# Kernel tuning notes

Measured on AMD Instinct MI355X. Metric: run time of the kernel, lower is better.

Reference implementation:

```python
import jax, jax.numpy as jnp
import numpy as np

EPS = 1e-6
TEMPERATURE = 0.1
NEG_INF = -1.0e9

B, S, H = 8, 1024, 1024
M = 16384  # memory_size


def setup_inputs() -> dict:
    key = jax.random.key(0)
    ks = jax.random.split(key, 10)
    sc = 1.0 / np.sqrt(H)
    return {
        "hidden_states": jax.random.normal(ks[0], (B, S, H), jnp.float32),
        "Wk": jax.random.normal(ks[1], (H, H), jnp.float32) * sc,
        "bk": jax.random.normal(ks[2], (H,), jnp.float32) * 0.01,
        "Wv": jax.random.normal(ks[3], (H, H), jnp.float32) * sc,
        "bv": jax.random.normal(ks[4], (H,), jnp.float32) * 0.01,
        "Wo": jax.random.normal(ks[5], (H, H), jnp.float32) * sc,
        "bo": jax.random.normal(ks[6], (H,), jnp.float32) * 0.01,
        "memory_keys": jax.random.normal(ks[7], (M, H), jnp.float32),
        "memory_values": jax.random.normal(ks[8], (M, H), jnp.float32),
        "memory_usage": jax.random.randint(ks[9], (M,), 0, 3, jnp.int32),
    }


def _normalize(x):
    # matches torch: x * rsqrt(sum(x^2) + 1e-6)
    return x * jax.lax.rsqrt(jnp.sum(jnp.square(x), axis=-1, keepdims=True) + EPS)


def reference(hidden_states, Wk, bk, Wv, bv, Wo, bo,
              memory_keys, memory_values, memory_usage):
    # key projection + L2-ish normalization of queries
    q = hidden_states @ Wk.T + bk              # [B,S,H]
    qn = _normalize(q)
    mkn = _normalize(memory_keys)              # [M,H]
    # cosine-similarity attention over memory slots
    scores = jnp.einsum('bsh,mh->bsm', qn, mkn) / TEMPERATURE  # [B,S,M]
    mask = (memory_usage > 0).astype(scores.dtype)             # [M]
    scores = scores * mask + NEG_INF * (1.0 - mask)
    w = jax.nn.softmax(scores, axis=-1)                        # [B,S,M]
    retrieved = jnp.einsum('bsm,mh->bsh', w, memory_values)    # [B,S,H]
    return retrieved @ Wo.T + bo
```

## Files before the change

kernel.cpp:

```cpp
#include <hip/hip_runtime.h>
#include <hip/hip_bf16.h>
#include <stdint.h>
#include <stddef.h>

typedef __bf16 bf16_t;
typedef __attribute__((ext_vector_type(8))) __bf16 bf16x8;
typedef __attribute__((ext_vector_type(4))) __bf16 bf16x4;
typedef __attribute__((ext_vector_type(4))) float f32x4;

#define HDIM 1024
#define MSLOTS 16384
#define NROWS 8192

__device__ __forceinline__ void load16_lds(const void* g, void* l) {
  __builtin_amdgcn_global_load_lds((const __attribute__((address_space(1))) void*)g,
                                   (__attribute__((address_space(3))) void*)l, 16, 0, 0);
}

__global__ void init_compact(int* __restrict__ cmask) {
  int i = blockIdx.x * blockDim.x + threadIdx.x;
  if (i < MSLOTS) cmask[i] = 0;
}

__global__ void compact_scan(const int* __restrict__ usage, int* __restrict__ posmap,
                             int* __restrict__ cmask, int* __restrict__ smalls) {
  __shared__ int wtot[16], wbase[16];
  const int t = threadIdx.x;
  const int lane = t & 63, wid = t >> 6;
  const int base = t * 16;
  unsigned mask = 0;
  int c = 0;
  #pragma unroll
  for (int i = 0; i < 16; ++i) {
    if (usage[base + i] > 0) { mask |= (1u << i); ++c; }
  }
  int inc = c;
  #pragma unroll
  for (int d = 1; d < 64; d <<= 1) {
    int n = __shfl_up(inc, d);
    if (lane >= d) inc += n;
  }
  if (lane == 63) wtot[wid] = inc;
  __syncthreads();
  if (t == 0) {
    int acc = 0;
    #pragma unroll
    for (int w = 0; w < 16; ++w) { wbase[w] = acc; acc += wtot[w]; }
    smalls[0] = acc;
    smalls[1] = ((acc + 511) >> 9) << 9;
  }
  __syncthreads();
  int pos = wbase[wid] + inc - c;
  #pragma unroll
  for (int i = 0; i < 16; ++i) {
    if ((mask >> i) & 1u) {
      posmap[pos] = base + i;
      cmask[pos] = 1;
      ++pos;
    }
  }
}

__global__ void cvt_f32_bf16(const float* __restrict__ X, bf16_t* __restrict__ Y, int n8) {
  int i = blockIdx.x * blockDim.x + threadIdx.x;
  if (i >= n8) return;
  float4 a = ((const float4*)X)[2 * i];
  float4 b = ((const float4*)X)[2 * i + 1];
  bf16x8 o;
  o[0] = (bf16_t)a.x; o[1] = (bf16_t)a.y; o[2] = (bf16_t)a.z; o[3] = (bf16_t)a.w;
  o[4] = (bf16_t)b.x; o[5] = (bf16_t)b.y; o[6] = (bf16_t)b.z; o[7] = (bf16_t)b.w;
  ((bf16x8*)Y)[i] = o;
}

__global__ void normalize_rows(const float* __restrict__ X, bf16_t* __restrict__ Y) {
  __shared__ float part[4];
  const int t = threadIdx.x;
  const size_t row = blockIdx.x;
  float4 v = ((const float4*)(X + row * 1024))[t];
  float s = v.x * v.x + v.y * v.y + v.z * v.z + v.w * v.w;
  #pragma unroll
  for (int m = 32; m >= 1; m >>= 1) s += __shfl_xor(s, m);
  if ((t & 63) == 0) part[t >> 6] = s;
  __syncthreads();
  float tot = part[0] + part[1] + part[2] + part[3];
  float r = rsqrtf(tot + 1e-6f);
  bf16x4 o;
  o[0] = (bf16_t)(v.x * r); o[1] = (bf16_t)(v.y * r);
  o[2] = (bf16_t)(v.z * r); o[3] = (bf16_t)(v.w * r);
  *(bf16x4*)&Y[row * 1024 + t * 4] = o;
}

__global__ void normalize_gather(const float* __restrict__ mk, const int* __restrict__ posmap,
                                 const int* __restrict__ smalls, bf16_t* __restrict__ cmkn) {
  __shared__ float part[4];
  const int p = blockIdx.x;
  const int cnt = smalls[0], mpad = smalls[1];
  if (p >= mpad) return;
  const int t = threadIdx.x;
  if (p >= cnt) {
    bf16x4 z;
    z[0] = z[1] = z[2] = z[3] = (bf16_t)0.f;
    *(bf16x4*)&cmkn[(size_t)p * 1024 + t * 4] = z;
    return;
  }
  const int slot = posmap[p];
  float4 v = ((const float4*)(mk + (size_t)slot * 1024))[t];
  float s = v.x * v.x + v.y * v.y + v.z * v.z + v.w * v.w;
  #pragma unroll
  for (int m = 32; m >= 1; m >>= 1) s += __shfl_xor(s, m);
  if ((t & 63) == 0) part[t >> 6] = s;
  __syncthreads();
  float tot = part[0] + part[1] + part[2] + part[3];
  float r = rsqrtf(tot + 1e-6f);
  bf16x4 o;
  o[0] = (bf16_t)(v.x * r); o[1] = (bf16_t)(v.y * r);
  o[2] = (bf16_t)(v.z * r); o[3] = (bf16_t)(v.w * r);
  *(bf16x4*)&cmkn[(size_t)p * 1024 + t * 4] = o;
}

__global__ void transpose_gather(const float* __restrict__ mv, const int* __restrict__ posmap,
                                 const int* __restrict__ smalls, bf16_t* __restrict__ cVt) {
  __shared__ float tile[32][33];
  const int cnt = smalls[0], mpad = smalls[1];
  const int p0 = blockIdx.y * 32;
  if (p0 >= mpad) return;
  const int tx = threadIdx.x & 31, ty = threadIdx.x >> 5;
  const int h0 = blockIdx.x * 32;
  #pragma unroll
  for (int j = 0; j < 32; j += 8) {
    const int pos = p0 + ty + j;
    float val = 0.f;
    if (pos < cnt) val = mv[(size_t)posmap[pos] * 1024 + h0 + tx];
    tile[ty + j][tx] = val;
  }
  __syncthreads();
  #pragma unroll
  for (int j = 0; j < 32; j += 8)
    cVt[(size_t)(h0 + ty + j) * MSLOTS + p0 + tx] = (bf16_t)tile[tx][ty + j];
}

__global__ void zero_f32(float* __restrict__ p, int n4) {
  int i = blockIdx.x * blockDim.x + threadIdx.x;
  if (i < n4) ((float4*)p)[i] = (float4){0.f, 0.f, 0.f, 0.f};
}

__global__ void scale_cvt(const float* __restrict__ retrf, const float* __restrict__ den,
                          bf16_t* __restrict__ out, int n4) {
  int i = blockIdx.x * blockDim.x + threadIdx.x;
  if (i >= n4) return;
  float4 s = ((const float4*)retrf)[i];
  const int row = (i * 4) >> 10;
  const float r = 1.0f / den[row];
  bf16x4 o;
  o[0] = (bf16_t)(s.x * r); o[1] = (bf16_t)(s.y * r);
  o[2] = (bf16_t)(s.z * r); o[3] = (bf16_t)(s.w * r);
  ((bf16x4*)out)[i] = o;
}

__global__ void reduce_scale(const float* __restrict__ part, size_t partStride, int ks,
                             const float* __restrict__ den, bf16_t* __restrict__ out, int n4) {
  int i = blockIdx.x * blockDim.x + threadIdx.x;
  if (i >= n4) return;
  float4 s = ((const float4*)part)[i];
  for (int k = 1; k < ks; ++k) {
    float4 t = ((const float4*)(part + (size_t)k * partStride))[i];
    s.x += t.x; s.y += t.y; s.z += t.z; s.w += t.w;
  }
  const int row = (i * 4) >> 10;
  const float r = 1.0f / den[row];
  bf16x4 o;
  o[0] = (bf16_t)(s.x * r); o[1] = (bf16_t)(s.y * r);
  o[2] = (bf16_t)(s.z * r); o[3] = (bf16_t)(s.w * r);
  ((bf16x4*)out)[i] = o;
}

template <int EPI>
__global__ __launch_bounds__(512, 2)
void gemm256(const bf16_t* __restrict__ A, const bf16_t* __restrict__ Bt,
             int ldk, int kLenIn, int ldc,
             const float* __restrict__ bias,
             const int* __restrict__ cmask,
             float* __restrict__ den,
             float* __restrict__ outf, bf16_t* __restrict__ outb,
             const int* __restrict__ smalls, int ks, size_t partStride) {
  __shared__ bf16_t lA[4][256 * 32];
  __shared__ bf16_t lB[4][256 * 32];
  const int tid = threadIdx.x;
  const int lane = tid & 63;
  const int wave = tid >> 6;
  const int wr = wave >> 2;
  const int wc = wave & 3;
  const int lr = lane & 15;
  const int lq = lane >> 4;

  int bx = blockIdx.x, by = blockIdx.y, bz = blockIdx.z;
  {
    const unsigned nx = gridDim.x, ny = gridDim.y;
    if ((ny & 7u) == 0u) {
      unsigned lin = blockIdx.x + nx * (blockIdx.y + ny * blockIdx.z);
      unsigned ylow = lin & 7u;
      lin >>= 3;
      const unsigned nyh = ny >> 3;
      unsigned yhigh = lin % nyh;
      lin /= nyh;
      bx = lin % nx;
      bz = lin / nx;
      by = ylow + 8u * yhigh;
    }
  }

  int kLen = kLenIn;
  int kstart = 0;
  if (EPI == 1) {
    if (bx * 256 >= smalls[1]) return;
  }
  if (EPI == 3 || EPI == 4) {
    kLen = smalls[1] / ks;
    kstart = bz * kLen;
  }
  const int nt = kLen >> 5;

  const int srow = tid >> 2;
  const int scol = (tid & 3) * 8;
  const bf16_t* pA0 = A + (size_t)(by * 256 + srow) * ldk + kstart + scol;
  const bf16_t* pA1 = pA0 + (size_t)128 * ldk;
  const bf16_t* pB0 = Bt + (size_t)(bx * 256 + srow) * ldk + kstart + scol;
  const bf16_t* pB1 = pB0 + (size_t)128 * ldk;

  f32x4 acc[8][4];
  #pragma unroll
  for (int m = 0; m < 8; ++m)
    #pragma unroll
    for (int n = 0; n < 4; ++n) acc[m][n] = (f32x4){0.f, 0.f, 0.f, 0.f};

#define STAGE(tt)                                              \
  do {                                                         \
    const int _b = (tt) & 3;                                   \
    const size_t _ko = (size_t)(tt) * 32;                      \
    load16_lds(pA0 + _ko, &lA[_b][tid * 8]);                   \
    load16_lds(pA1 + _ko, &lA[_b][4096 + tid * 8]);            \
    load16_lds(pB0 + _ko, &lB[_b][tid * 8]);                   \
    load16_lds(pB1 + _ko, &lB[_b][4096 + tid * 8]);            \
  } while (0)

  if (nt > 0) STAGE(0);
  if (nt > 1) STAGE(1);
  if (nt > 2) STAGE(2);

  for (int t = 0; t < nt; ++t) {
    if (t + 3 < nt) STAGE(t + 3);
    const int rem = nt - 1 - t;
    if (rem >= 3)      asm volatile("s_waitcnt vmcnt(12)" ::: "memory");
    else if (rem == 2) asm volatile("s_waitcnt vmcnt(8)" ::: "memory");
    else if (rem == 1) asm volatile("s_waitcnt vmcnt(4)" ::: "memory");
    else               asm volatile("s_waitcnt vmcnt(0)" ::: "memory");
    __builtin_amdgcn_s_barrier();
    __builtin_amdgcn_sched_barrier(0);
    const int b = t & 3;
    const bf16_t* bAp = &lA[b][0];
    const bf16_t* bBp = &lB[b][0];
    bf16x8 bfr[4];
    #pragma unroll
    for (int n = 0; n < 4; ++n)
      bfr[n] = *(const bf16x8*)&bBp[(wc * 64 + n * 16 + lr) * 32 + lq * 8];
    __builtin_amdgcn_s_setprio(1);
    #pragma unroll
    for (int m = 0; m < 8; ++m) {
      bf16x8 af = *(const bf16x8*)&bAp[(wr * 128 + m * 16 + lr) * 32 + lq * 8];
      #pragma unroll
      for (int n = 0; n < 4; ++n)
        acc[m][n] = __builtin_amdgcn_mfma_f32_16x16x32_bf16(af, bfr[n], acc[m][n], 0, 0, 0);
    }
    __builtin_amdgcn_s_setprio(0);
    __builtin_amdgcn_sched_barrier(0);
    __builtin_amdgcn_s_barrier();
    __builtin_amdgcn_sched_barrier(0);
  }
#undef STAGE

  const int colBase = bx * 256 + wc * 64 + lr;
  const int rowBase = by * 256 + wr * 128 + lq * 4;

  if (EPI == 1) {
    bool ok[4];
    #pragma unroll
    for (int n = 0; n < 4; ++n) ok[n] = cmask[colBase + n * 16] > 0;
    #pragma unroll
    for (int m = 0; m < 8; ++m) {
      #pragma unroll
      for (int r = 0; r < 4; ++r) {
        const int row = rowBase + m * 16 + r;
        float s = 0.f;
        #pragma unroll
        for (int n = 0; n < 4; ++n) {
          float e = ok[n] ? exp2f(acc[m][n][r] * 14.426950408889634f) : 0.f;
          s += e;
          outb[(size_t)row * ldc + colBase + n * 16] = (bf16_t)e;
        }
        s += __shfl_xor(s, 1);
        s += __shfl_xor(s, 2);
        s += __shfl_xor(s, 4);
        s += __shfl_xor(s, 8);
        if (lr == 0) atomicAdd(&den[row], s);
      }
    }
  }
  if (EPI == 3 || EPI == 4) {
    if (EPI == 4) outf += (size_t)bz * partStride;
    #pragma unroll
    for (int m = 0; m < 8; ++m)
      #pragma unroll
      for (int n = 0; n < 4; ++n)
        #pragma unroll
        for (int r = 0; r < 4; ++r) {
          const size_t idx = (size_t)(rowBase + m * 16 + r) * ldc + colBase + n * 16;
          if (EPI == 3) atomicAdd(&outf[idx], acc[m][n][r]);
          else outf[idx] = acc[m][n][r];
        }
  }
}

template <int EPI>
__global__ void gemm_bt(const bf16_t* __restrict__ A, const bf16_t* __restrict__ Bt,
                        int ldk, int kLenIn, int ldc,
                        const float* __restrict__ bias,
                        const int* __restrict__ cmask,
                        float* __restrict__ den,
                        float* __restrict__ outf, bf16_t* __restrict__ outb,
                        const int* __restrict__ smalls, int ks, size_t partStride) {
  __shared__ bf16_t lA[128 * 32];
  __shared__ bf16_t lB[128 * 32];
  const int t = threadIdx.x;
  const int lane = t & 63;
  const int wave = t >> 6;
  const int wm = (wave >> 1) << 6;
  const int wn = (wave & 1) << 6;
  const int lr = lane & 15;
  const int lq = lane >> 4;

  int bx = blockIdx.x, by = blockIdx.y, bz = blockIdx.z;
  {
    const unsigned nx = gridDim.x, ny = gridDim.y;
    if ((ny & 7u) == 0u) {
      unsigned lin = blockIdx.x + nx * (blockIdx.y + ny * blockIdx.z);
      unsigned ylow = lin & 7u;
      lin >>= 3;
      const unsigned nyh = ny >> 3;
      unsigned yhigh = lin % nyh;
      lin /= nyh;
      bx = lin % nx;
      bz = lin / nx;
      by = ylow + 8u * yhigh;
    }
  }

  int kLen = kLenIn;
  int kstart = 0;

  const int r0 = t >> 2;
  const int c0 = (t & 3) * 8;
  const bf16_t* pA0 = A + (size_t)(by * 128 + r0) * ldk + kstart + c0;
  const bf16_t* pA1 = pA0 + (size_t)64 * ldk;
  const bf16_t* pB0 = Bt + (size_t)(bx * 128 + r0) * ldk + kstart + c0;
  const bf16_t* pB1 = pB0 + (size_t)64 * ldk;

  f32x4 acc[4][4];
  #pragma unroll
  for (int i = 0; i < 4; ++i)
    #pragma unroll
    for (int j = 0; j < 4; ++j) acc[i][j] = (f32x4){0.f, 0.f, 0.f, 0.f};

  for (int k0 = 0; k0 < kLen; k0 += 32) {
    __syncthreads();
    load16_lds(pA0, &lA[t * 8]);
    load16_lds(pA1, &lA[2048 + t * 8]);
    load16_lds(pB0, &lB[t * 8]);
    load16_lds(pB1, &lB[2048 + t * 8]);
    pA0 += 32; pA1 += 32; pB0 += 32; pB1 += 32;
    __syncthreads();
    bf16x8 af[4], bfr[4];
    #pragma unroll
    for (int i = 0; i < 4; ++i)
      af[i] = *(const bf16x8*)&lA[(wm + i * 16 + lr) * 32 + lq * 8];
    #pragma unroll
    for (int j = 0; j < 4; ++j)
      bfr[j] = *(const bf16x8*)&lB[(wn + j * 16 + lr) * 32 + lq * 8];
    #pragma unroll
    for (int i = 0; i < 4; ++i)
      #pragma unroll
      for (int j = 0; j < 4; ++j)
        acc[i][j] = __builtin_amdgcn_mfma_f32_16x16x32_bf16(af[i], bfr[j], acc[i][j], 0, 0, 0);
  }

  const int colBase = bx * 128 + wn + lr;
  const int rowBase = by * 128 + wm + lq * 4;

  #pragma unroll
  for (int j = 0; j < 4; ++j) {
    const int col = colBase + j * 16;
    float bval = 0.f;
    if (EPI == 0) bval = bias[col];
    #pragma unroll
    for (int i = 0; i < 4; ++i) {
      const int row = rowBase + i * 16;
      #pragma unroll
      for (int r = 0; r < 4; ++r) {
        const size_t idx = (size_t)(row + r) * ldc + col;
        float v = acc[i][j][r];
        if (EPI == 0) outf[idx] = v + bval;
      }
    }
  }
}

extern "C" void kernel_launch(void* const* d_in, const int* in_sizes, int n_in,
                              void* d_out, int out_size, void* d_ws, size_t ws_size,
                              hipStream_t stream) {
  const float* hs = (const float*)d_in[0];
  const float* Wk = (const float*)d_in[1];
  const float* bk = (const float*)d_in[2];
  const float* Wo = (const float*)d_in[5];
  const float* bo = (const float*)d_in[6];
  const float* mk = (const float*)d_in[7];
  const float* mv = (const float*)d_in[8];
  const int* usage = (const int*)d_in[9];
  float* out = (float*)d_out;

  char* ws = (char*)d_ws;
  size_t off = 0;
  auto alloc = [&](size_t b) -> void* {
    void* p = ws + off;
    off += (b + 255) & ~(size_t)255;
    return p;
  };
  bf16_t* cmkn = (bf16_t*)alloc((size_t)MSLOTS * HDIM * 2);
  bf16_t* cVt = (bf16_t*)alloc((size_t)HDIM * MSLOTS * 2);
  bf16_t* qnb = (bf16_t*)alloc((size_t)NROWS * HDIM * 2);
  bf16_t* retrb = (bf16_t*)alloc((size_t)NROWS * HDIM * 2);
  bf16_t* Wob = (bf16_t*)alloc((size_t)HDIM * HDIM * 2);
  float* den = (float*)alloc((size_t)NROWS * 4);
  int* posmap = (int*)alloc((size_t)MSLOTS * 4);
  int* cmask = (int*)alloc((size_t)MSLOTS * 4);
  int* smalls = (int*)alloc(256 * 4);
  const size_t fixed = off;

  int chunk = 256, ksplit = 4, partialMode = 0;
  {
    const int cc[8] = {4096, 4096, 2048, 2048, 1024, 1024, 512, 256};
    const int kk[8] = {4, 4, 8, 8, 8, 8, 16, 4};
    const int pp[8] = {1, 0, 1, 0, 1, 0, 0, 0};
    for (int ci = 0; ci < 8; ++ci) {
      size_t outBytes = pp[ci] ? (size_t)cc[ci] * HDIM * 4 * kk[ci] : (size_t)cc[ci] * HDIM * 4;
      size_t region = (size_t)cc[ci] * MSLOTS * 2 + outBytes;
      size_t phaseA = (size_t)NROWS * HDIM * 2 + (size_t)HDIM * HDIM * 2 +
                      (size_t)NROWS * HDIM * 4 + 1024;
      if (region < phaseA) region = phaseA;
      if (fixed + region <= ws_size) {
        chunk = cc[ci]; ksplit = kk[ci]; partialMode = pp[ci];
        break;
      }
    }
  }
  bf16_t* hsb = (bf16_t*)(ws + fixed);
  bf16_t* Wkb = (bf16_t*)(ws + fixed + (size_t)NROWS * HDIM * 2);
  float* qf = (float*)(ws + fixed + (size_t)NROWS * HDIM * 2 + (size_t)HDIM * HDIM * 2);
  bf16_t* P = (bf16_t*)(ws + fixed);
  float* retrf = (float*)(ws + fixed + (size_t)chunk * MSLOTS * 2);
  const size_t partStride = (size_t)chunk * HDIM;

  init_compact<<<MSLOTS / 256, 256, 0, stream>>>(cmask);
  compact_scan<<<1, 1024, 0, stream>>>(usage, posmap, cmask, smalls);
  cvt_f32_bf16<<<(NROWS * HDIM / 8 + 255) / 256, 256, 0, stream>>>(hs, hsb, NROWS * HDIM / 8);
  cvt_f32_bf16<<<(HDIM * HDIM / 8 + 255) / 256, 256, 0, stream>>>(Wk, Wkb, HDIM * HDIM / 8);
  cvt_f32_bf16<<<(HDIM * HDIM / 8 + 255) / 256, 256, 0, stream>>>(Wo, Wob, HDIM * HDIM / 8);
  normalize_gather<<<MSLOTS, 256, 0, stream>>>(mk, posmap, smalls, cmkn);
  transpose_gather<<<dim3(HDIM / 32, MSLOTS / 32), 256, 0, stream>>>(mv, posmap, smalls, cVt);

  gemm_bt<0><<<dim3(HDIM / 128, NROWS / 128), 256, 0, stream>>>(
      hsb, Wkb, HDIM, HDIM, HDIM, bk, nullptr, nullptr, qf, nullptr, smalls, 1, 0);
  normalize_rows<<<NROWS, 256, 0, stream>>>(qf, qnb);

  for (int c = 0; c < NROWS; c += chunk) {
    zero_f32<<<(chunk / 4 + 255) / 256, 256, 0, stream>>>(den, chunk / 4);
    gemm256<1><<<dim3(MSLOTS / 256, chunk / 256), 512, 0, stream>>>(
        qnb + (size_t)c * HDIM, cmkn, HDIM, HDIM, MSLOTS, nullptr, cmask, den, nullptr, P,
        smalls, 1, 0);
    if (partialMode) {
      gemm256<4><<<dim3(HDIM / 256, chunk / 256, ksplit), 512, 0, stream>>>(
          P, cVt, MSLOTS, 0, HDIM, nullptr, nullptr, nullptr, retrf, nullptr, smalls, ksplit,
          partStride);
      reduce_scale<<<(chunk * HDIM / 4 + 255) / 256, 256, 0, stream>>>(
          retrf, partStride, ksplit, den, retrb + (size_t)c * HDIM, chunk * HDIM / 4);
    } else {
      zero_f32<<<(chunk * HDIM / 4 + 255) / 256, 256, 0, stream>>>(retrf, chunk * HDIM / 4);
      gemm256<3><<<dim3(HDIM / 256, chunk / 256, ksplit), 512, 0, stream>>>(
          P, cVt, MSLOTS, 0, HDIM, nullptr, nullptr, nullptr, retrf, nullptr, smalls, ksplit,
          0);
      scale_cvt<<<(chunk * HDIM / 4 + 255) / 256, 256, 0, stream>>>(
          retrf, den, retrb + (size_t)c * HDIM, chunk * HDIM / 4);
    }
  }

  gemm_bt<0><<<dim3(HDIM / 128, NROWS / 128), 256, 0, stream>>>(
      retrb, Wob, HDIM, HDIM, HDIM, bo, nullptr, nullptr, out, nullptr, smalls, 1, 0);
}
```

Measured before the change: 918.7 us.

## Restructure gemm256 main loop to K=64 double-buffered LDS with XOR swizzle

Rewrites the 256x256 MFMA GEMM main loop. The old version used a 4-deep ring of K=32 slices; the new one uses two K=64 buffers, splits each iteration into four quarter-phases, and issues the next tile's loads between compute steps. It also XOR-swizzles the LDS layout to cut bank conflicts on the ds_read path, and lowers the k-split for chunk 512. The aim is fewer barriers per FLOP and fewer LDS conflicts, at the cost of more barriers per iteration and added dependence on the K length being a multiple of 64. gemm_bt is also cleaned up by dropping its template and unused parameters.

```diff
diff --git a/kernel.cpp b/kernel.cpp
--- a/kernel.cpp
+++ b/kernel.cpp
@@ -174,17 +174,59 @@
   ((bf16x4*)out)[i] = o;
 }
 
+#define SB __builtin_amdgcn_sched_barrier(0)
+
+#define STAGE(TT, HF)                                                          \
+  {                                                                            \
+    const int isB_ = ((HF) < 2) ? 1 : 0;                                       \
+    const int h_ = (HF) & 1;                                                   \
+    bf16_t* d_ = &sm[(TT) & 1][isB_][h_ * 8192 + tid * 8];                     \
+    const bf16_t* s_ = (isB_ ? pBstg : pAstg) + (size_t)h_ * 128 * ldk +       \
+                       (size_t)(kstart + ((TT) << 6));                         \
+    load16_lds(s_, d_);                                                        \
+    load16_lds(s_ + (size_t)64 * ldk, d_ + 4096);                              \
+  }
+
+#define RDA(Q)                                                                 \
+  {                                                                            \
+    _Pragma("unroll") for (int m2 = 0; m2 < 2; ++m2)                           \
+      _Pragma("unroll") for (int kk = 0; kk < 2; ++kk) {                       \
+        const int r_ = (Q) * 64 + wr * 32 + m2 * 16 + lr;                      \
+        const int sg_ = kk * 4 + lq;                                           \
+        af[m2 * 2 + kk] =                                                      \
+            *(const bf16x8*)(bA + r_ * 128 + ((sg_ ^ (r_ & 7)) << 4));         \
+      }                                                                        \
+  }
+
+#define RDB()                                                                  \
+  {                                                                            \
+    _Pragma("unroll") for (int n = 0; n < 4; ++n)                              \
+      _Pragma("unroll") for (int kk = 0; kk < 2; ++kk) {                       \
+        const int r_ = wc * 64 + n * 16 + lr;                                  \
+        const int sg_ = kk * 4 + lq;                                           \
+        bfr[n * 2 + kk] =                                                      \
+            *(const bf16x8*)(bB + r_ * 128 + ((sg_ ^ (r_ & 7)) << 4));         \
+      }                                                                        \
+  }
+
+#define MFQ(Q)                                                                 \
+  {                                                                            \
+    _Pragma("unroll") for (int m2 = 0; m2 < 2; ++m2)                           \
+      _Pragma("unroll") for (int n = 0; n < 4; ++n)                            \
+        _Pragma("unroll") for (int kk = 0; kk < 2; ++kk)                       \
+          acc[(Q) * 2 + m2][n] = __builtin_amdgcn_mfma_f32_16x16x32_bf16(      \
+              af[m2 * 2 + kk], bfr[n * 2 + kk], acc[(Q) * 2 + m2][n], 0, 0, 0);\
+  }
+
 template <int EPI>
 __global__ __launch_bounds__(512, 2)
 void gemm256(const bf16_t* __restrict__ A, const bf16_t* __restrict__ Bt,
              int ldk, int kLenIn, int ldc,
-             const float* __restrict__ bias,
              const int* __restrict__ cmask,
              float* __restrict__ den,
              float* __restrict__ outf, bf16_t* __restrict__ outb,
              const int* __restrict__ smalls, int ks, size_t partStride) {
-  __shared__ bf16_t lA[4][256 * 32];
-  __shared__ bf16_t lB[4][256 * 32];
+  __shared__ bf16_t sm[2][2][256 * 64];
   const int tid = threadIdx.x;
   const int lane = tid & 63;
   const int wave = tid >> 6;
@@ -218,14 +260,12 @@
     kLen = smalls[1] / ks;
     kstart = bz * kLen;
   }
-  const int nt = kLen >> 5;
-
-  const int srow = tid >> 2;
-  const int scol = (tid & 3) * 8;
-  const bf16_t* pA0 = A + (size_t)(by * 256 + srow) * ldk + kstart + scol;
-  const bf16_t* pA1 = pA0 + (size_t)128 * ldk;
-  const bf16_t* pB0 = Bt + (size_t)(bx * 256 + srow) * ldk + kstart + scol;
-  const bf16_t* pB1 = pB0 + (size_t)128 * ldk;
+  const int nt = kLen >> 6;
+  if (nt <= 0) return;
+
+  const size_t stgOff = (size_t)(tid >> 3) * ldk + (((tid & 7) ^ ((tid >> 3) & 7)) << 3);
+  const bf16_t* pAstg = A + (size_t)(by * 256) * ldk + stgOff;
+  const bf16_t* pBstg = Bt + (size_t)(bx * 256) * ldk + stgOff;
 
   f32x4 acc[8][4];
   #pragma unroll
@@ -233,53 +273,41 @@
     #pragma unroll
     for (int n = 0; n < 4; ++n) acc[m][n] = (f32x4){0.f, 0.f, 0.f, 0.f};
 
-#define STAGE(tt)                                              \
-  do {                                                         \
-    const int _b = (tt) & 3;                                   \
-    const size_t _ko = (size_t)(tt) * 32;                      \
-    load16_lds(pA0 + _ko, &lA[_b][tid * 8]);                   \
-    load16_lds(pA1 + _ko, &lA[_b][4096 + tid * 8]);            \
-    load16_lds(pB0 + _ko, &lB[_b][tid * 8]);                   \
-    load16_lds(pB1 + _ko, &lB[_b][4096 + tid * 8]);            \
-  } while (0)
-
-  if (nt > 0) STAGE(0);
-  if (nt > 1) STAGE(1);
-  if (nt > 2) STAGE(2);
+  bf16x8 af[4], bfr[8];
+
+  STAGE(0, 0); STAGE(0, 1); STAGE(0, 2); STAGE(0, 3);
 
   for (int t = 0; t < nt; ++t) {
-    if (t + 3 < nt) STAGE(t + 3);
-    const int rem = nt - 1 - t;
-    if (rem >= 3)      asm volatile("s_waitcnt vmcnt(12)" ::: "memory");
-    else if (rem == 2) asm volatile("s_waitcnt vmcnt(8)" ::: "memory");
-    else if (rem == 1) asm volatile("s_waitcnt vmcnt(4)" ::: "memory");
-    else               asm volatile("s_waitcnt vmcnt(0)" ::: "memory");
-    __builtin_amdgcn_s_barrier();
-    __builtin_amdgcn_sched_barrier(0);
-    const int b = t & 3;
-    const bf16_t* bAp = &lA[b][0];
-    const bf16_t* bBp = &lB[b][0];
-    bf16x8 bfr[4];
-    #pragma unroll
-    for (int n = 0; n < 4; ++n)
-      bfr[n] = *(const bf16x8*)&bBp[(wc * 64 + n * 16 + lr) * 32 + lq * 8];
-    __builtin_amdgcn_s_setprio(1);
-    #pragma unroll
-    for (int m = 0; m < 8; ++m) {
-      bf16x8 af = *(const bf16x8*)&bAp[(wr * 128 + m * 16 + lr) * 32 + lq * 8];
-      #pragma unroll
-      for (int n = 0; n < 4; ++n)
-        acc[m][n] = __builtin_amdgcn_mfma_f32_16x16x32_bf16(af, bfr[n], acc[m][n], 0, 0, 0);
-    }
-    __builtin_amdgcn_s_setprio(0);
-    __builtin_amdgcn_sched_barrier(0);
-    __builtin_amdgcn_s_barrier();
-    __builtin_amdgcn_sched_barrier(0);
-  }
-#undef STAGE
+    const char* bA = (const char*)sm[t & 1][0];
+    const char* bB = (const char*)sm[t & 1][1];
+    const bool more = (t + 1 < nt);
+
+    asm volatile("s_waitcnt vmcnt(2)" ::: "memory");
+    SB; __builtin_amdgcn_s_barrier(); SB;
+    if (more) STAGE(t + 1, 0);
+    RDB();
+    RDA(0);
+    __builtin_amdgcn_s_setprio(1); MFQ(0); __builtin_amdgcn_s_setprio(0); SB;
+
+    __builtin_amdgcn_s_barrier(); SB;
+    if (more) STAGE(t + 1, 1);
+    RDA(1);
+    __builtin_amdgcn_s_setprio(1); MFQ(1); __builtin_amdgcn_s_setprio(0); SB;
+
+    if (more) { asm volatile("s_waitcnt vmcnt(4)" ::: "memory"); }
+    else      { asm volatile("s_waitcnt vmcnt(0)" ::: "memory"); }
+    SB; __builtin_amdgcn_s_barrier(); SB;
+    if (more) STAGE(t + 1, 2);
+    RDA(2);
+    __builtin_amdgcn_s_setprio(1); MFQ(2); __builtin_amdgcn_s_setprio(0); SB;
+
+    __builtin_amdgcn_s_barrier(); SB;
+    if (more) STAGE(t + 1, 3);
+    RDA(3);
+    __builtin_amdgcn_s_setprio(1); MFQ(3); __builtin_amdgcn_s_setprio(0); SB;
+  }
 
   const int colBase = bx * 256 + wc * 64 + lr;
-  const int rowBase = by * 256 + wr * 128 + lq * 4;
 
   if (EPI == 1) {
     bool ok[4];
@@ -287,9 +315,10 @@
     for (int n = 0; n < 4; ++n) ok[n] = cmask[colBase + n * 16] > 0;
     #pragma unroll
     for (int m = 0; m < 8; ++m) {
+      const int row0 = by * 256 + (m >> 1) * 64 + wr * 32 + (m & 1) * 16 + lq * 4;
       #pragma unroll
       for (int r = 0; r < 4; ++r) {
-        const int row = rowBase + m * 16 + r;
+        const int row = row0 + r;
         float s = 0.f;
         #pragma unroll
         for (int n = 0; n < 4; ++n) {
@@ -308,26 +337,24 @@
   if (EPI == 3 || EPI == 4) {
     if (EPI == 4) outf += (size_t)bz * partStride;
     #pragma unroll
-    for (int m = 0; m < 8; ++m)
+    for (int m = 0; m < 8; ++m) {
+      const int row0 = by * 256 + (m >> 1) * 64 + wr * 32 + (m & 1) * 16 + lq * 4;
       #pragma unroll
       for (int n = 0; n < 4; ++n)
         #pragma unroll
         for (int r = 0; r < 4; ++r) {
-          const size_t idx = (size_t)(rowBase + m * 16 + r) * ldc + colBase + n * 16;
+          const size_t idx = (size_t)(row0 + r) * ldc + colBase + n * 16;
           if (EPI == 3) atomicAdd(&outf[idx], acc[m][n][r]);
           else outf[idx] = acc[m][n][r];
         }
-  }
-}
-
-template <int EPI>
+    }
+  }
+}
+
 __global__ void gemm_bt(const bf16_t* __restrict__ A, const bf16_t* __restrict__ Bt,
                         int ldk, int kLenIn, int ldc,
                         const float* __restrict__ bias,
-                        const int* __restrict__ cmask,
-                        float* __restrict__ den,
-                        float* __restrict__ outf, bf16_t* __restrict__ outb,
-                        const int* __restrict__ smalls, int ks, size_t partStride) {
+                        float* __restrict__ outf) {
   __shared__ bf16_t lA[128 * 32];
   __shared__ bf16_t lB[128 * 32];
   const int t = threadIdx.x;
@@ -338,30 +365,27 @@
   const int lr = lane & 15;
   const int lq = lane >> 4;
 
-  int bx = blockIdx.x, by = blockIdx.y, bz = blockIdx.z;
+  int bx = blockIdx.x, by = blockIdx.y;
   {
     const unsigned nx = gridDim.x, ny = gridDim.y;
     if ((ny & 7u) == 0u) {
-      unsigned lin = blockIdx.x + nx * (blockIdx.y + ny * blockIdx.z);
+      unsigned lin = blockIdx.x + nx * blockIdx.y;
       unsigned ylow = lin & 7u;
       lin >>= 3;
       const unsigned nyh = ny >> 3;
       unsigned yhigh = lin % nyh;
       lin /= nyh;
       bx = lin % nx;
-      bz = lin / nx;
       by = ylow + 8u * yhigh;
     }
   }
 
-  int kLen = kLenIn;
-  int kstart = 0;
-
+  const int kLen = kLenIn;
   const int r0 = t >> 2;
   const int c0 = (t & 3) * 8;
-  const bf16_t* pA0 = A + (size_t)(by * 128 + r0) * ldk + kstart + c0;
+  const bf16_t* pA0 = A + (size_t)(by * 128 + r0) * ldk + c0;
   const bf16_t* pA1 = pA0 + (size_t)64 * ldk;
-  const bf16_t* pB0 = Bt + (size_t)(bx * 128 + r0) * ldk + kstart + c0;
+  const bf16_t* pB0 = Bt + (size_t)(bx * 128 + r0) * ldk + c0;
   const bf16_t* pB1 = pB0 + (size_t)64 * ldk;
 
   f32x4 acc[4][4];
@@ -378,18 +402,18 @@
     load16_lds(pB1, &lB[2048 + t * 8]);
     pA0 += 32; pA1 += 32; pB0 += 32; pB1 += 32;
     __syncthreads();
-    bf16x8 af[4], bfr[4];
+    bf16x8 af[4], bfv[4];
     #pragma unroll
     for (int i = 0; i < 4; ++i)
       af[i] = *(const bf16x8*)&lA[(wm + i * 16 + lr) * 32 + lq * 8];
     #pragma unroll
     for (int j = 0; j < 4; ++j)
-      bfr[j] = *(const bf16x8*)&lB[(wn + j * 16 + lr) * 32 + lq * 8];
+      bfv[j] = *(const bf16x8*)&lB[(wn + j * 16 + lr) * 32 + lq * 8];
     #pragma unroll
     for (int i = 0; i < 4; ++i)
       #pragma unroll
       for (int j = 0; j < 4; ++j)
-        acc[i][j] = __builtin_amdgcn_mfma_f32_16x16x32_bf16(af[i], bfr[j], acc[i][j], 0, 0, 0);
+        acc[i][j] = __builtin_amdgcn_mfma_f32_16x16x32_bf16(af[i], bfv[j], acc[i][j], 0, 0, 0);
   }
 
   const int colBase = bx * 128 + wn + lr;
@@ -398,17 +422,13 @@
   #pragma unroll
   for (int j = 0; j < 4; ++j) {
     const int col = colBase + j * 16;
-    float bval = 0.f;
-    if (EPI == 0) bval = bias[col];
+    const float bval = bias[col];
     #pragma unroll
     for (int i = 0; i < 4; ++i) {
       const int row = rowBase + i * 16;
       #pragma unroll
-      for (int r = 0; r < 4; ++r) {
-        const size_t idx = (size_t)(row + r) * ldc + col;
-        float v = acc[i][j][r];
-        if (EPI == 0) outf[idx] = v + bval;
-      }
+      for (int r = 0; r < 4; ++r)
+        outf[(size_t)(row + r) * ldc + col] = acc[i][j][r] + bval;
     }
   }
 }
@@ -447,7 +467,7 @@
   int chunk = 256, ksplit = 4, partialMode = 0;
   {
     const int cc[8] = {4096, 4096, 2048, 2048, 1024, 1024, 512, 256};
-    const int kk[8] = {4, 4, 8, 8, 8, 8, 16, 4};
+    const int kk[8] = {4, 4, 8, 8, 8, 8, 8, 4};
     const int pp[8] = {1, 0, 1, 0, 1, 0, 0, 0};
     for (int ci = 0; ci < 8; ++ci) {
       size_t outBytes = pp[ci] ? (size_t)cc[ci] * HDIM * 4 * kk[ci] : (size_t)cc[ci] * HDIM * 4;
@@ -476,31 +496,31 @@
   normalize_gather<<<MSLOTS, 256, 0, stream>>>(mk, posmap, smalls, cmkn);
   transpose_gather<<<dim3(HDIM / 32, MSLOTS / 32), 256, 0, stream>>>(mv, posmap, smalls, cVt);
 
-  gemm_bt<0><<<dim3(HDIM / 128, NROWS / 128), 256, 0, stream>>>(
-      hsb, Wkb, HDIM, HDIM, HDIM, bk, nullptr, nullptr, qf, nullptr, smalls, 1, 0);
+  gemm_bt<<<dim3(HDIM / 128, NROWS / 128), 256, 0, stream>>>(
+      hsb, Wkb, HDIM, HDIM, HDIM, bk, qf);
   normalize_rows<<<NROWS, 256, 0, stream>>>(qf, qnb);
 
   for (int c = 0; c < NROWS; c += chunk) {
     zero_f32<<<(chunk / 4 + 255) / 256, 256, 0, stream>>>(den, chunk / 4);
     gemm256<1><<<dim3(MSLOTS / 256, chunk / 256), 512, 0, stream>>>(
-        qnb + (size_t)c * HDIM, cmkn, HDIM, HDIM, MSLOTS, nullptr, cmask, den, nullptr, P,
+        qnb + (size_t)c * HDIM, cmkn, HDIM, HDIM, MSLOTS, cmask, den, nullptr, P,
         smalls, 1, 0);
     if (partialMode) {
       gemm256<4><<<dim3(HDIM / 256, chunk / 256, ksplit), 512, 0, stream>>>(
-          P, cVt, MSLOTS, 0, HDIM, nullptr, nullptr, nullptr, retrf, nullptr, smalls, ksplit,
+          P, cVt, MSLOTS, 0, HDIM, nullptr, nullptr, retrf, nullptr, smalls, ksplit,
           partStride);
       reduce_scale<<<(chunk * HDIM / 4 + 255) / 256, 256, 0, stream>>>(
           retrf, partStride, ksplit, den, retrb + (size_t)c * HDIM, chunk * HDIM / 4);
     } else {
       zero_f32<<<(chunk * HDIM / 4 + 255) / 256, 256, 0, stream>>>(retrf, chunk * HDIM / 4);
       gemm256<3><<<dim3(HDIM / 256, chunk / 256, ksplit), 512, 0, stream>>>(
-          P, cVt, MSLOTS, 0, HDIM, nullptr, nullptr, nullptr, retrf, nullptr, smalls, ksplit,
+          P, cVt, MSLOTS, 0, HDIM, nullptr, nullptr, retrf, nullptr, smalls, ksplit,
           0);
       scale_cvt<<<(chunk * HDIM / 4 + 255) / 256, 256, 0, stream>>>(
           retrf, den, retrb + (size_t)c * HDIM, chunk * HDIM / 4);
     }
   }
 
-  gemm_bt<0><<<dim3(HDIM / 128, NROWS / 128), 256, 0, stream>>>(
-      retrb, Wob, HDIM, HDIM, HDIM, bo, nullptr, nullptr, out, nullptr, smalls, 1, 0);
-}
+  gemm_bt<<<dim3(HDIM / 128, NROWS / 128), 256, 0, stream>>>(
+      retrb, Wob, HDIM, HDIM, HDIM, bo, out);
+}
```

New measurement: 796.7 us. 1.15x faster.
